# Kernel tuning notes

Hardware: AMD Instinct MI355X
Metric: run time of the kernel (lower is better)

Reference implementation:

```python
import jax, jax.numpy as jnp
import numpy as np

N, E, H, FN, FE, FO, L = 20000, 50000, 32, 4, 2, 4, 3

def _gelu(v):
    return jax.nn.gelu(v, approximate=False)  # torch nn.GELU default = exact erf

def setup_inputs() -> dict:
    key = jax.random.key(0)
    ks = jax.random.split(key, 24)
    def w(k, shape, fan_in):
        return jax.random.normal(k, shape, dtype=jnp.float32) / np.sqrt(fan_in)
    inp = {
        "x": jax.random.normal(ks[0], (N, FN), dtype=jnp.float32),
        "pred_mask": (jax.random.uniform(ks[1], (N, FN)) < 0.5).astype(jnp.float32),
        "edge_index": jax.random.randint(ks[2], (2, E), 0, N, dtype=jnp.int64),
        "edge_attr": jax.random.normal(ks[3], (E, FE), dtype=jnp.float32),
        # input encoder
        "W_in": w(ks[4], (FN, H), FN), "b_in": jnp.zeros((H,), jnp.float32),
        # mask embedding MLP
        "mW1": w(ks[5], (FN, H), FN), "mb1": jnp.zeros((H,), jnp.float32),
        "mW2": w(ks[6], (H, H), H),   "mb2": jnp.zeros((H,), jnp.float32),
        # per-layer stacked params (leading dim L)
        "eW1": w(ks[7], (L, FE, H), FE),    "eb1": jnp.zeros((L, H), jnp.float32),
        "eW2": w(ks[8], (L, H, H * H), H),  "eb2": jnp.zeros((L, H * H), jnp.float32),
        "W_root": w(ks[9], (L, H, H), H),   "conv_b": jnp.zeros((L, H), jnp.float32),
        "gamma": jnp.ones((L, H), jnp.float32), "beta": jnp.zeros((L, H), jnp.float32),
        # output decoder
        "dW1": w(ks[10], (H, H), H),  "db1": jnp.zeros((H,), jnp.float32),
        "dW2": w(ks[11], (H, FO), H), "db2": jnp.zeros((FO,), jnp.float32),
    }
    return inp

def reference(x, pred_mask, edge_index, edge_attr,
              W_in, b_in, mW1, mb1, mW2, mb2,
              eW1, eb1, eW2, eb2, W_root, conv_b, gamma, beta,
              dW1, db1, dW2, db2):
    # input projection + mask embedding
    h = x @ W_in + b_in + (_gelu(pred_mask @ mW1 + mb1) @ mW2 + mb2)
    # undirect graph (random edge list is directed -> torch path duplicates)
    src = jnp.concatenate([edge_index[0], edge_index[1]])  # [2E]
    dst = jnp.concatenate([edge_index[1], edge_index[0]])
    ea = jnp.concatenate([edge_attr, edge_attr], axis=0)    # [2E, FE]

    def layer(h, p):
        w1, b1, w2, b2, wr, cb, g, b = p
        # edge-conditioned weights: [2E, H, H]
        ew = (_gelu(ea @ w1 + b1) @ w2 + b2).reshape(-1, H, H)
        msg = jnp.einsum('eh,eho->eo', h[src], ew)          # gather + per-edge matvec
        agg = jax.ops.segment_sum(msg, dst, num_segments=N) # scatter-add
        hc = agg + h @ wr + cb                               # NNConv root weight + bias
        mu = jnp.mean(hc, axis=-1, keepdims=True)
        var = jnp.var(hc, axis=-1, keepdims=True)
        hn = (hc - mu) * jax.lax.rsqrt(var + 1e-5) * g + b   # LayerNorm
        return h + _gelu(hn), None                           # dropout in eval mode (no-op)

    h, _ = jax.lax.scan(layer, h, (eW1, eb1, eW2, eb2, W_root, conv_b, gamma, beta))
    out = _gelu(h @ dW1 + db1) @ dW2 + db2
    return out
```

## Files before the change

### kernel.cpp

```cpp
#include <hip/hip_runtime.h>
#include <hip/hip_bf16.h>
#include <math.h>

#define NN  20000
#define NE  50000
#define NE2 100000
#define H   32
#define FN  4
#define FE  2
#define FO  4
#define NL  3

#define FRAGS_PER_LAYER (33 * 2)
#define BVALS_PER_LAYER (FRAGS_PER_LAYER * 512)

#define NB_PREP ((NL * BVALS_PER_LAYER + 255)/256)
#define NB_ZERO (NN * H / 4 / 256)
#define NB_ENC  ((NN + 255)/256)

#define TCHUNKS 196
#define EB      256

typedef __attribute__((ext_vector_type(8))) short short8;
typedef __attribute__((ext_vector_type(4))) float f32x4;
typedef __attribute__((ext_vector_type(4))) unsigned int u32x4;

__device__ __forceinline__ float gelu_f(float x) {
    return 0.5f * x * (1.0f + erff(x * 0.7071067811865476f));
}
__device__ __forceinline__ short f2bf(float x) {
    __hip_bfloat16 b = __float2bfloat16(x);
    return __builtin_bit_cast(short, b);
}
__device__ __forceinline__ unsigned int cvt_pk_bf16(float lo, float hi) {
    unsigned int r;
    asm("v_cvt_pk_bf16_f32 %0, %1, %2" : "=v"(r) : "v"(lo), "v"(hi));
    return r;
}

__global__ __launch_bounds__(256) void prologue(
    const float* __restrict__ x, const float* __restrict__ pm,
    const float* __restrict__ W_in, const float* __restrict__ b_in,
    const float* __restrict__ mW1, const float* __restrict__ mb1,
    const float* __restrict__ mW2, const float* __restrict__ mb2,
    const float* __restrict__ eW2, const float* __restrict__ eb2,
    float* __restrict__ h, float* __restrict__ agg,
    short* __restrict__ Bhi)
{
    int bid = blockIdx.x;
    int tid = threadIdx.x;

    if (bid < NB_PREP) {
        int idx = bid * 256 + tid;
        if (idx >= NL * BVALS_PER_LAYER) return;
        int layer = idx / BVALS_PER_LAYER;
        int rem   = idx - layer * BVALS_PER_LAYER;
        int f      = rem >> 9;
        int within = rem & 511;
        int step = f >> 1, nt = f & 1;
        int l = within >> 3, j = within & 7;
        int p = ((l >> 4) << 3) + j;
        int n = nt * 16 + (l & 15);
        float v;
        if (step < 32) v = eW2[layer * 32768 + step * 1024 + p * 32 + n];
        else           v = eb2[layer * 1024 + p * 32 + n];
        Bhi[idx] = f2bf(v);
        return;
    }
    bid -= NB_PREP;

    if (bid < NB_ZERO) {
        int i = bid * 256 + tid;
        ((float4*)agg)[i] = make_float4(0.f, 0.f, 0.f, 0.f);
        return;
    }
    bid -= NB_ZERO;

    __shared__ float sWin[FN*H], sW1[FN*H], sW2[H*H];
    __shared__ float sbin[H], sb1[H], sb2[H];
    for (int i = tid; i < FN*H; i += 256) { sWin[i] = W_in[i]; sW1[i] = mW1[i]; }
    for (int i = tid; i < H*H; i += 256) sW2[i] = mW2[i];
    if (tid < H) { sbin[tid] = b_in[tid]; sb1[tid] = mb1[tid]; sb2[tid] = mb2[tid]; }
    __syncthreads();
    int n = bid * 256 + tid;
    if (n >= NN) return;
    float xv[FN], pv[FN];
#pragma unroll
    for (int i = 0; i < FN; ++i) { xv[i] = x[n*FN+i]; pv[i] = pm[n*FN+i]; }
    float m[H];
#pragma unroll
    for (int j = 0; j < H; ++j) {
        float a = sb1[j];
#pragma unroll
        for (int i = 0; i < FN; ++i) a += pv[i] * sW1[i*H+j];
        m[j] = gelu_f(a);
    }
#pragma unroll
    for (int j = 0; j < H; ++j) {
        float a = sbin[j] + sb2[j];
#pragma unroll
        for (int i = 0; i < FN; ++i) a += xv[i] * sWin[i*H+j];
        float s = 0.f;
#pragma unroll
        for (int k = 0; k < H; ++k) s += m[k] * sW2[k*H+j];
        h[n*H+j] = a + s;
    }
}

__global__ __launch_bounds__(256) void edge_pass(
    const float* __restrict__ h,
    const int* __restrict__ ei,
    const float* __restrict__ ea,
    const float* __restrict__ w1,
    const float* __restrict__ b1,
    const short* __restrict__ Bhi,
    float* __restrict__ agg)
{
    __shared__ float t_lds[32][EB];
    __shared__ int src_lds[EB], dst_lds[EB];
    __shared__ float sw[3*H];

    int tid = threadIdx.x;
    int bid = blockIdx.x;
    bool half2 = bid >= TCHUNKS;
    int er_base = (half2 ? bid - TCHUNKS : bid) * EB;

    if (tid < H) {
        sw[tid]       = w1[tid];
        sw[H + tid]   = w1[H + tid];
        sw[2*H + tid] = b1[tid];
    }
    {
        int er = er_base + tid;
        int erc = er < NE ? er : NE - 1;
        int s, d;
        if (half2) { s = ei[NE + erc]; d = ei[erc]; }
        else       { s = ei[erc];      d = ei[NE + erc]; }
        bool v = er < NE;
        src_lds[tid] = v ? s : 0;
        dst_lds[tid] = v ? d : 0;
    }
    __syncthreads();

    {
        int er = er_base + tid;
        int erc = er < NE ? er : NE - 1;
        float2 av = *(const float2*)(ea + (size_t)erc * 2);
#pragma unroll 8
        for (int k = 0; k < 32; ++k) {
            t_lds[k][tid] = gelu_f(av.x * sw[k] + av.y * sw[H + k] + sw[2*H + k]);
        }
    }
    __syncthreads();

    int wv = tid >> 6, lane = tid & 63;
    int lg = lane >> 4, lm = lane & 15;
    int jbase = wv * 64;

    float hs[4][8];
#pragma unroll
    for (int m = 0; m < 4; ++m) {
        int s = src_lds[jbase + m*16 + lm];
        const float4* hp = (const float4*)(h + (size_t)s*H + lg*8);
        float4 u0 = hp[0], u1 = hp[1];
        hs[m][0]=u0.x; hs[m][1]=u0.y; hs[m][2]=u0.z; hs[m][3]=u0.w;
        hs[m][4]=u1.x; hs[m][5]=u1.y; hs[m][6]=u1.z; hs[m][7]=u1.w;
    }

    f32x4 acc[4][2];
#pragma unroll
    for (int m = 0; m < 4; ++m) {
        acc[m][0] = (f32x4){0.f,0.f,0.f,0.f};
        acc[m][1] = (f32x4){0.f,0.f,0.f,0.f};
    }

    const short8* F = (const short8*)Bhi;
    short8 A0 = F[lane],        A1 = F[64 + lane];
    short8 B0 = F[128 + lane],  B1 = F[192 + lane];
    short8 C0, C1;

#pragma unroll 1
    for (int step = 0; step < 32; ++step) {
        if (step + 2 <= 32) {
            int fo = (step + 2) * 128 + lane;
            C0 = F[fo]; C1 = F[fo + 64];
        }
#pragma unroll
        for (int m = 0; m < 4; ++m) {
            float tv = t_lds[step][jbase + m*16 + lm];
            u32x4 pr;
            pr[0] = cvt_pk_bf16(tv * hs[m][0], tv * hs[m][1]);
            pr[1] = cvt_pk_bf16(tv * hs[m][2], tv * hs[m][3]);
            pr[2] = cvt_pk_bf16(tv * hs[m][4], tv * hs[m][5]);
            pr[3] = cvt_pk_bf16(tv * hs[m][6], tv * hs[m][7]);
            short8 a = __builtin_bit_cast(short8, pr);
            acc[m][0] = __builtin_amdgcn_mfma_f32_16x16x32_bf16(a, A0, acc[m][0], 0, 0, 0);
            acc[m][1] = __builtin_amdgcn_mfma_f32_16x16x32_bf16(a, A1, acc[m][1], 0, 0, 0);
        }
        A0 = B0; A1 = B1; B0 = C0; B1 = C1;
    }
#pragma unroll
    for (int m = 0; m < 4; ++m) {
        u32x4 pr;
        pr[0] = cvt_pk_bf16(hs[m][0], hs[m][1]);
        pr[1] = cvt_pk_bf16(hs[m][2], hs[m][3]);
        pr[2] = cvt_pk_bf16(hs[m][4], hs[m][5]);
        pr[3] = cvt_pk_bf16(hs[m][6], hs[m][7]);
        short8 a = __builtin_bit_cast(short8, pr);
        acc[m][0] = __builtin_amdgcn_mfma_f32_16x16x32_bf16(a, A0, acc[m][0], 0, 0, 0);
        acc[m][1] = __builtin_amdgcn_mfma_f32_16x16x32_bf16(a, A1, acc[m][1], 0, 0, 0);
    }

#pragma unroll
    for (int m = 0; m < 4; ++m) {
#pragma unroll
        for (int r = 0; r < 4; ++r) {
            int erow = jbase + m*16 + lg*4 + r;
            if (er_base + erow < NE) {
                int d = dst_lds[erow];
                atomicAdd(agg + (size_t)d*H + lm,      acc[m][0][r]);
                atomicAdd(agg + (size_t)d*H + 16 + lm, acc[m][1][r]);
            }
        }
    }
}

__global__ __launch_bounds__(256) void node_update(
    float* __restrict__ h, float* __restrict__ agg,
    const float* __restrict__ wr, const float* __restrict__ cb,
    const float* __restrict__ gamma, const float* __restrict__ beta,
    const float* __restrict__ dW1, const float* __restrict__ db1,
    const float* __restrict__ dW2, const float* __restrict__ db2,
    float* __restrict__ out, int last)
{
    __shared__ float swr[H*H], sW1d[H*H], sW2d[H*FO];
    __shared__ float scb[H], sg[H], sb[H], sb1d[H], sb2d[FO];
    int tid = threadIdx.x;
    for (int i = tid; i < H*H; i += 256) { swr[i] = wr[i]; sW1d[i] = dW1[i]; }
    for (int i = tid; i < H*FO; i += 256) sW2d[i] = dW2[i];
    if (tid < H) { scb[tid] = cb[tid]; sg[tid] = gamma[tid]; sb[tid] = beta[tid]; sb1d[tid] = db1[tid]; }
    if (tid < FO) sb2d[tid] = db2[tid];
    __syncthreads();
    int n = blockIdx.x * 256 + tid;
    if (n >= NN) return;

    float hv[H], hc[H];
#pragma unroll
    for (int q = 0; q < 8; ++q) {
        float4 v = ((const float4*)(h + n*H))[q];
        hv[q*4+0]=v.x; hv[q*4+1]=v.y; hv[q*4+2]=v.z; hv[q*4+3]=v.w;
        float4 g = ((const float4*)(agg + n*H))[q];
        hc[q*4+0]=g.x; hc[q*4+1]=g.y; hc[q*4+2]=g.z; hc[q*4+3]=g.w;
    }
#pragma unroll
    for (int o = 0; o < H; ++o) hc[o] += scb[o];
#pragma unroll
    for (int k = 0; k < H; ++k) {
        float hk = hv[k];
#pragma unroll
        for (int o = 0; o < H; ++o) hc[o] += hk * swr[k*H+o];
    }
    float mu = 0.f;
#pragma unroll
    for (int o = 0; o < H; ++o) mu += hc[o];
    mu *= (1.0f/H);
    float var = 0.f;
#pragma unroll
    for (int o = 0; o < H; ++o) { float d = hc[o]-mu; var += d*d; }
    var *= (1.0f/H);
    float rs = rsqrtf(var + 1e-5f);
#pragma unroll
    for (int o = 0; o < H; ++o) {
        float hn = (hc[o]-mu)*rs*sg[o] + sb[o];
        hv[o] += gelu_f(hn);
    }

    if (!last) {
#pragma unroll
        for (int q = 0; q < 8; ++q) {
            ((float4*)(h + n*H))[q]   = make_float4(hv[q*4+0], hv[q*4+1], hv[q*4+2], hv[q*4+3]);
            ((float4*)(agg + n*H))[q] = make_float4(0.f, 0.f, 0.f, 0.f);
        }
    } else {
        float g[H];
#pragma unroll
        for (int j = 0; j < H; ++j) {
            float a = sb1d[j];
#pragma unroll
            for (int k = 0; k < H; ++k) a += hv[k] * sW1d[k*H+j];
            g[j] = gelu_f(a);
        }
#pragma unroll
        for (int o = 0; o < FO; ++o) {
            float a = sb2d[o];
#pragma unroll
            for (int k = 0; k < H; ++k) a += g[k] * sW2d[k*FO+o];
            out[n*FO+o] = a;
        }
    }
}

extern "C" void kernel_launch(void* const* d_in, const int* in_sizes, int n_in,
                              void* d_out, int out_size, void* d_ws, size_t ws_size,
                              hipStream_t stream)
{
    const float* x    = (const float*)d_in[0];
    const float* pm   = (const float*)d_in[1];
    const int*   ei   = (const int*)d_in[2];
    const float* ea   = (const float*)d_in[3];
    const float* W_in = (const float*)d_in[4];
    const float* b_in = (const float*)d_in[5];
    const float* mW1  = (const float*)d_in[6];
    const float* mb1  = (const float*)d_in[7];
    const float* mW2  = (const float*)d_in[8];
    const float* mb2  = (const float*)d_in[9];
    const float* eW1  = (const float*)d_in[10];
    const float* eb1  = (const float*)d_in[11];
    const float* eW2  = (const float*)d_in[12];
    const float* eb2  = (const float*)d_in[13];
    const float* Wr   = (const float*)d_in[14];
    const float* cb   = (const float*)d_in[15];
    const float* gm   = (const float*)d_in[16];
    const float* bt   = (const float*)d_in[17];
    const float* dW1  = (const float*)d_in[18];
    const float* db1  = (const float*)d_in[19];
    const float* dW2  = (const float*)d_in[20];
    const float* db2  = (const float*)d_in[21];
    float* out = (float*)d_out;

    float* h   = (float*)d_ws;
    float* agg = h + NN*H;
    short* Bhi = (short*)(agg + NN*H);

    prologue<<<NB_PREP + NB_ZERO + NB_ENC, 256, 0, stream>>>(
        x, pm, W_in, b_in, mW1, mb1, mW2, mb2, eW2, eb2, h, agg, Bhi);

    for (int l = 0; l < NL; ++l) {
        edge_pass<<<2*TCHUNKS, 256, 0, stream>>>(
            h, ei, ea, eW1 + l*FE*H, eb1 + l*H,
            Bhi + l*BVALS_PER_LAYER, agg);
        node_update<<<(NN + 255)/256, 256, 0, stream>>>(
            h, agg, Wr + l*H*H, cb + l*H, gm + l*H, bt + l*H,
            dW1, db1, dW2, db2, out, l == NL-1);
    }
}
```

Baseline: 151.6 us.

## Process both edge directions per block to share edge-attribute MLP work

```diff
diff --git a/kernel.cpp b/kernel.cpp
--- a/kernel.cpp
+++ b/kernel.cpp
@@ -18,8 +18,8 @@
 #define NB_ZERO (NN * H / 4 / 256)
 #define NB_ENC  ((NN + 255)/256)
 
-#define TCHUNKS 196
-#define EB      256
+#define EPB     64
+#define NB_EDGE ((NE + EPB - 1) / EPB)
 
 typedef __attribute__((ext_vector_type(8))) short short8;
 typedef __attribute__((ext_vector_type(4))) float f32x4;
@@ -107,7 +107,7 @@
     }
 }
 
-__global__ __launch_bounds__(256) void edge_pass(
+__global__ __launch_bounds__(128) void edge_pass(
     const float* __restrict__ h,
     const int* __restrict__ ei,
     const float* __restrict__ ea,
@@ -116,39 +116,38 @@
     const short* __restrict__ Bhi,
     float* __restrict__ agg)
 {
-    __shared__ float t_lds[32][EB];
-    __shared__ int src_lds[EB], dst_lds[EB];
+    __shared__ float t_lds[32][EPB];
+    __shared__ int src_lds[2*EPB], dst_lds[2*EPB];
     __shared__ float sw[3*H];
 
     int tid = threadIdx.x;
     int bid = blockIdx.x;
-    bool half2 = bid >= TCHUNKS;
-    int er_base = (half2 ? bid - TCHUNKS : bid) * EB;
-
-    if (tid < H) {
-        sw[tid]       = w1[tid];
-        sw[H + tid]   = w1[H + tid];
-        sw[2*H + tid] = b1[tid];
-    }
+    int er_base = bid * EPB;
+
+    if (tid < 2*H)      sw[tid] = w1[tid];
+    else if (tid < 3*H) sw[tid] = b1[tid - 2*H];
+
     {
-        int er = er_base + tid;
+        int e  = tid & 63;
+        int er = er_base + e;
         int erc = er < NE ? er : NE - 1;
-        int s, d;
-        if (half2) { s = ei[NE + erc]; d = ei[erc]; }
-        else       { s = ei[erc];      d = ei[NE + erc]; }
-        bool v = er < NE;
-        src_lds[tid] = v ? s : 0;
-        dst_lds[tid] = v ? d : 0;
+        int a0 = ei[erc], a1 = ei[NE + erc];
+        bool fwd = tid < 64;
+        src_lds[tid] = fwd ? a0 : a1;
+        dst_lds[tid] = fwd ? a1 : a0;
     }
     __syncthreads();
 
     {
-        int er = er_base + tid;
+        int e  = tid & 63;
+        int kq = tid >> 6;
+        int er = er_base + e;
         int erc = er < NE ? er : NE - 1;
         float2 av = *(const float2*)(ea + (size_t)erc * 2);
-#pragma unroll 8
-        for (int k = 0; k < 32; ++k) {
-            t_lds[k][tid] = gelu_f(av.x * sw[k] + av.y * sw[H + k] + sw[2*H + k]);
+#pragma unroll
+        for (int kk = 0; kk < 16; ++kk) {
+            int k = kq * 16 + kk;
+            t_lds[k][e] = gelu_f(av.x * sw[k] + av.y * sw[H + k] + sw[2*H + k]);
         }
     }
     __syncthreads();
@@ -187,7 +186,7 @@
         }
 #pragma unroll
         for (int m = 0; m < 4; ++m) {
-            float tv = t_lds[step][jbase + m*16 + lm];
+            float tv = t_lds[step][m*16 + lm];
             u32x4 pr;
             pr[0] = cvt_pk_bf16(tv * hs[m][0], tv * hs[m][1]);
             pr[1] = cvt_pk_bf16(tv * hs[m][2], tv * hs[m][3]);
@@ -215,9 +214,9 @@
     for (int m = 0; m < 4; ++m) {
 #pragma unroll
         for (int r = 0; r < 4; ++r) {
-            int erow = jbase + m*16 + lg*4 + r;
-            if (er_base + erow < NE) {
-                int d = dst_lds[erow];
+            int j = jbase + m*16 + lg*4 + r;
+            if (er_base + (j & 63) < NE) {
+                int d = dst_lds[j];
                 atomicAdd(agg + (size_t)d*H + lm,      acc[m][0][r]);
                 atomicAdd(agg + (size_t)d*H + 16 + lm, acc[m][1][r]);
             }
@@ -336,7 +335,7 @@
         x, pm, W_in, b_in, mW1, mb1, mW2, mb2, eW2, eb2, h, agg, Bhi);
 
     for (int l = 0; l < NL; ++l) {
-        edge_pass<<<2*TCHUNKS, 256, 0, stream>>>(
+        edge_pass<<<NB_EDGE, 128, 0, stream>>>(
             h, ei, ea, eW1 + l*FE*H, eb1 + l*H,
             Bhi + l*BVALS_PER_LAYER, agg);
         node_update<<<(NN + 255)/256, 256, 0, stream>>>(
```

Result: slower. 155.4 us (+2.5%).
